# Kernel tuning notes

Hardware: AMD Instinct MI355X
Metric: run time of the kernel (lower is better)

## Reference

```python
import jax, jax.numpy as jnp
import numpy as np

DIM, HEADS, DIM_HEAD = 1024, 16, 64
INNER = HEADS * DIM_HEAD
EPS = 1e-5

def layernorm(x, w, b):
    mu = jnp.mean(x, axis=-1, keepdims=True)
    var = jnp.var(x, axis=-1, keepdims=True)
    return (x - mu) / jnp.sqrt(var + EPS) * w + b

def setup_inputs() -> dict:
    key = jax.random.key(0)
    ks = jax.random.split(key, 8)
    s = lambda d: 1.0 / np.sqrt(d)
    return {
        'x': jax.random.normal(ks[0], (4, 2048, DIM), jnp.float32),
        'media': jax.random.normal(ks[1], (4, 1024, DIM), jnp.float32),
        'ln_w': jnp.ones((DIM,), jnp.float32),
        'ln_b': jnp.zeros((DIM,), jnp.float32),
        'Wq': jax.random.normal(ks[2], (DIM, INNER), jnp.float32) * s(DIM),
        'Wkv': jax.random.normal(ks[3], (DIM, 2 * INNER), jnp.float32) * s(DIM),
        'Wo': jax.random.normal(ks[4], (INNER, DIM), jnp.float32) * s(INNER),
        'attn_gate': jnp.zeros((1,), jnp.float32),
        'ffln_w': jnp.ones((DIM,), jnp.float32),
        'ffln_b': jnp.zeros((DIM,), jnp.float32),
        'W1': jax.random.normal(ks[5], (DIM, 4 * DIM), jnp.float32) * s(DIM),
        'W2': jax.random.normal(ks[6], (4 * DIM, DIM), jnp.float32) * s(4 * DIM),
    }

def reference(x, media, ln_w, ln_b, Wq, Wkv, Wo, attn_gate, ffln_w, ffln_b, W1, W2):
    scale = DIM_HEAD ** (-0.5)
    b, n, _ = x.shape
    m = media.shape[1]
    # MaskedCrossAttention
    xn = layernorm(x, ln_w, ln_b)
    q = (xn @ Wq).reshape(b, n, HEADS, DIM_HEAD).transpose(0, 2, 1, 3)  # b h n d
    kv = media @ Wkv
    k, v = jnp.split(kv, 2, axis=-1)
    k = k.reshape(b, m, HEADS, DIM_HEAD).transpose(0, 2, 1, 3)  # b h m d
    v = v.reshape(b, m, HEADS, DIM_HEAD).transpose(0, 2, 1, 3)
    sim = jnp.einsum('bhid,bhjd->bhij', q * scale, k)
    # original subtracts detached row-max then softmax: identical to stable softmax
    attn = jax.nn.softmax(sim, axis=-1)
    out = jnp.einsum('bhij,bhjd->bhid', attn, v)
    out = out.transpose(0, 2, 1, 3).reshape(b, n, INNER) @ Wo
    x = out * jnp.tanh(attn_gate) + x
    # FeedForward (note: ff_gate exists in module but is unused in forward)
    h = layernorm(x, ffln_w, ffln_b) @ W1
    h = jax.nn.gelu(h, approximate=False) @ W2
    return h + x
```

## Files before the change

### kernel.cpp

```cpp
#include <hip/hip_runtime.h>
#include <hip/hip_bf16.h>

using bf16 = __hip_bfloat16;
typedef __attribute__((ext_vector_type(8))) short short8;
typedef __attribute__((ext_vector_type(4))) float f32x4;

typedef const void __attribute__((address_space(1))) gvoid;
typedef void __attribute__((address_space(3))) svoid;

__device__ __forceinline__ f32x4 mfma16(short8 a, short8 b, f32x4 c) {
    return __builtin_amdgcn_mfma_f32_16x16x32_bf16(a, b, c, 0, 0, 0);
}

__device__ __forceinline__ void async16(void* lds, const void* g) {
    __builtin_amdgcn_global_load_lds((gvoid*)g, (svoid*)lds, 16, 0, 0);
}

__device__ __forceinline__ unsigned short f2b(float f) {
    bf16 h = __float2bfloat16(f);
    unsigned short u;
    __builtin_memcpy(&u, &h, 2);
    return u;
}

__device__ __forceinline__ float fast_gelu(float x) {
    const float z0 = fmaf(x * x * x, 0.1029432f, 2.3022083f * x);
    const float z = fminf(z0, 80.0f);
    const float e = __builtin_amdgcn_exp2f(z);
    return x * e / (1.0f + e);
}

__global__ __launch_bounds__(256) void prep(
    const float* __restrict__ Wq, const float* __restrict__ Wkv,
    const float* __restrict__ Wo, const float* __restrict__ W1,
    const float* __restrict__ W2, bf16* __restrict__ WqT, bf16* __restrict__ WkvT,
    bf16* __restrict__ WoT, bf16* __restrict__ W1T, bf16* __restrict__ W2T,
    const float* __restrict__ media, bf16* __restrict__ mediab,
    const float* __restrict__ gate, float* __restrict__ gatet) {
    int id = blockIdx.x;
    const float* in;
    bf16* outp;
    int K, N, bx, by;
    if (id < 1024) {
        in = Wq; outp = WqT; K = 1024; N = 1024; bx = id & 31; by = id >> 5;
    } else if (id < 3072) {
        id -= 1024; in = Wkv; outp = WkvT; K = 1024; N = 2048; bx = id & 63; by = id >> 6;
    } else if (id < 4096) {
        id -= 3072; in = Wo; outp = WoT; K = 1024; N = 1024; bx = id & 31; by = id >> 5;
    } else if (id < 8192) {
        id -= 4096; in = W1; outp = W1T; K = 1024; N = 4096; bx = id & 127; by = id >> 7;
    } else if (id < 12288) {
        id -= 8192; in = W2; outp = W2T; K = 4096; N = 1024; bx = id & 31; by = id >> 5;
    } else {
        if (blockIdx.x == 12288 && threadIdx.x == 0) gatet[0] = tanhf(gate[0]);
        id -= 12288;
        const size_t i = (size_t)id * 256 + threadIdx.x;
        float4 v = ((const float4*)media)[i];
        ushort4 o;
        o.x = f2b(v.x); o.y = f2b(v.y); o.z = f2b(v.z); o.w = f2b(v.w);
        ((ushort4*)mediab)[i] = o;
        return;
    }
    __shared__ float tile[32][33];
    const int tx = threadIdx.x & 31, ty = threadIdx.x >> 5;
    const int n0 = bx * 32, k0 = by * 32;
#pragma unroll
    for (int j = 0; j < 32; j += 8)
        tile[ty + j][tx] = in[(size_t)(k0 + ty + j) * N + n0 + tx];
    __syncthreads();
#pragma unroll
    for (int j = 0; j < 32; j += 8)
        outp[(size_t)(n0 + ty + j) * K + k0 + tx] = __float2bfloat16(tile[tx][ty + j]);
}

__global__ __launch_bounds__(256) void layernorm_bf16(
    const float* __restrict__ x, const float* __restrict__ w,
    const float* __restrict__ b, bf16* __restrict__ out) {
    const int row = blockIdx.x, t = threadIdx.x;
    const float4 v = ((const float4*)(x + (size_t)row * 1024))[t];
    float s = v.x + v.y + v.z + v.w;
    float s2 = v.x * v.x + v.y * v.y + v.z * v.z + v.w * v.w;
#pragma unroll
    for (int off = 1; off < 64; off <<= 1) {
        s += __shfl_xor(s, off);
        s2 += __shfl_xor(s2, off);
    }
    __shared__ float rs[4], rs2[4];
    if ((t & 63) == 0) { rs[t >> 6] = s; rs2[t >> 6] = s2; }
    __syncthreads();
    const float S = rs[0] + rs[1] + rs[2] + rs[3];
    const float S2 = rs2[0] + rs2[1] + rs2[2] + rs2[3];
    const float mean = S * (1.0f / 1024.0f);
    const float var = S2 * (1.0f / 1024.0f) - mean * mean;
    const float rstd = rsqrtf(var + 1e-5f);
    const float4 wv = ((const float4*)w)[t];
    const float4 bv = ((const float4*)b)[t];
    ushort4 o;
    o.x = f2b((v.x - mean) * rstd * wv.x + bv.x);
    o.y = f2b((v.y - mean) * rstd * wv.y + bv.y);
    o.z = f2b((v.z - mean) * rstd * wv.z + bv.z);
    o.w = f2b((v.w - mean) * rstd * wv.w + bv.w);
    ((ushort4*)(out + (size_t)row * 1024))[t] = o;
}

__global__ __launch_bounds__(256) void vtranspose(
    const bf16* __restrict__ kvb, bf16* __restrict__ vtg) {
    const int mt = blockIdx.x, bh = blockIdx.y;
    const int b = bh >> 4, h = bh & 15;
    const int m0 = mt * 64;
    __shared__ bf16 tile[64 * 72];
    const int t = threadIdx.x;
#pragma unroll
    for (int i = 0; i < 2; ++i) {
        const int m = i * 32 + (t >> 3);
        short8 v = *(const short8*)(kvb + ((size_t)b * 1024 + m0 + m) * 2048 + 1024 +
                                    (size_t)h * 64 + (t & 7) * 8);
        *(short8*)&tile[m * 72 + (t & 7) * 8] = v;
    }
    __syncthreads();
#pragma unroll
    for (int i = 0; i < 2; ++i) {
        const int d = i * 32 + (t >> 3);
        const int mb = (t & 7) * 8;
        bf16 tmp[8];
#pragma unroll
        for (int j = 0; j < 8; ++j) tmp[j] = tile[(mb + j) * 72 + d];
        *(short8*)(vtg + (size_t)bh * 65536 + (size_t)d * 1024 + m0 + mb) = *(short8*)tmp;
    }
}

enum { EPI_BF16 = 0, EPI_GELU = 1, EPI_GATE_RES = 2, EPI_RES = 3 };

template <int EPI>
__global__ __launch_bounds__(256) void gemm_bf16(
    const bf16* __restrict__ A, const bf16* __restrict__ BT, void* __restrict__ Cout,
    const float* __restrict__ res, const float* __restrict__ gate_p,
    int M, int N, int K) {
    __shared__ bf16 As[128 * 64];
    __shared__ bf16 Bs[128 * 64];
    const int t = threadIdx.x;
    const int lane = t & 63;
    const int quad = lane >> 4, l15 = lane & 15;
    const int wave = t >> 6;
    const int wm = (wave >> 1) * 64, wn = (wave & 1) * 64;
    const int bm = blockIdx.x * 128, bn = blockIdx.y * 128;

    const int sr = t >> 3;
    const int sc = (t & 7) ^ (sr & 7);
    const bf16* Ag = A + (size_t)(bm + sr) * K + sc * 8;
    const bf16* Bg = BT + (size_t)(bn + sr) * K + sc * 8;

    f32x4 acc[4][4] = {};

    for (int k0 = 0; k0 < K; k0 += 64) {
#pragma unroll
        for (int i = 0; i < 4; ++i) {
            async16(&As[i * 2048 + t * 8], Ag + (size_t)i * 32 * K + k0);
            async16(&Bs[i * 2048 + t * 8], Bg + (size_t)i * 32 * K + k0);
        }
        __syncthreads();

#pragma unroll
        for (int dk = 0; dk < 2; ++dk) {
            short8 af[4], bf[4];
#pragma unroll
            for (int i = 0; i < 4; ++i)
                af[i] = *(const short8*)&As[(wm + i * 16 + l15) * 64 +
                                            (((dk * 4 + quad) ^ (l15 & 7)) * 8)];
#pragma unroll
            for (int i = 0; i < 4; ++i)
                bf[i] = *(const short8*)&Bs[(wn + i * 16 + l15) * 64 +
                                            (((dk * 4 + quad) ^ (l15 & 7)) * 8)];
#pragma unroll
            for (int i = 0; i < 4; ++i)
#pragma unroll
                for (int j = 0; j < 4; ++j)
                    acc[i][j] = mfma16(af[i], bf[j], acc[i][j]);
        }
        __syncthreads();
    }

    const float gate = (EPI == EPI_GATE_RES) ? gate_p[0] : 0.0f;
#pragma unroll
    for (int i = 0; i < 4; ++i) {
#pragma unroll
        for (int j = 0; j < 4; ++j) {
#pragma unroll
            for (int r = 0; r < 4; ++r) {
                const int row = bm + wm + i * 16 + quad * 4 + r;
                const int col = bn + wn + j * 16 + l15;
                const size_t idx = (size_t)row * N + col;
                const float v = acc[i][j][r];
                if constexpr (EPI == EPI_BF16) {
                    ((bf16*)Cout)[idx] = __float2bfloat16(v);
                } else if constexpr (EPI == EPI_GELU) {
                    ((bf16*)Cout)[idx] = __float2bfloat16(fast_gelu(v));
                } else if constexpr (EPI == EPI_GATE_RES) {
                    ((float*)Cout)[idx] = gate * v + res[idx];
                } else {
                    ((float*)Cout)[idx] = v + res[idx];
                }
            }
        }
    }
}

__global__ __launch_bounds__(256) void attention(
    const bf16* __restrict__ q, const bf16* __restrict__ kvb,
    const bf16* __restrict__ vtg, bf16* __restrict__ out) {
    const int bh = blockIdx.y;
    const int b = bh >> 4, h = bh & 15;
    const int t = threadIdx.x;
    const int wave = t >> 6, lane = t & 63;
    const int quad = lane >> 4, l15 = lane & 15;
    const int qrow0 = blockIdx.x * 128 + wave * 32;

    __shared__ bf16 Ks[128 * 64];
    __shared__ bf16 Vts[64 * 128];
    __shared__ bf16 Ps[4][16 * 128];

    short8 qa[2][2];
    const size_t qbase = ((size_t)b * 2048 + qrow0) * 1024 + (size_t)h * 64;
#pragma unroll
    for (int g = 0; g < 2; ++g)
#pragma unroll
        for (int dk = 0; dk < 2; ++dk)
            qa[g][dk] = *(const short8*)(q + qbase + (size_t)(g * 16 + l15) * 1024 + dk * 32 + quad * 8);

    f32x4 o[2][4] = {};
    float lsum[2][4] = {};

    const int km = t >> 3;
    const int kc = (t & 7) ^ (km & 7);
    const bf16* ksrc = kvb + ((size_t)b * 1024 + km) * 2048 + (size_t)h * 64 + kc * 8;
    const int vd = t >> 4;
    const int vc = (t & 15) ^ vd;
    const bf16* vsrc = vtg + (size_t)bh * 65536 + (size_t)vd * 1024 + vc * 8;

    bf16* Pw = &Ps[wave][0];

    for (int m0 = 0; m0 < 1024; m0 += 128) {
        __syncthreads();
#pragma unroll
        for (int i = 0; i < 4; ++i) {
            async16(&Ks[i * 2048 + t * 8], ksrc + ((size_t)m0 + i * 32) * 2048);
            async16(&Vts[i * 2048 + t * 8], vsrc + (size_t)i * 16 * 1024 + m0);
        }
        __syncthreads();

#pragma unroll
        for (int g = 0; g < 2; ++g) {
#pragma unroll
            for (int mt = 0; mt < 8; ++mt) {
                f32x4 s = {};
#pragma unroll
                for (int dk = 0; dk < 2; ++dk) {
                    short8 kb = *(const short8*)&Ks[(mt * 16 + l15) * 64 +
                                                    (((dk * 4 + quad) ^ (l15 & 7)) * 8)];
                    s = mfma16(qa[g][dk], kb, s);
                }
                const int pc = mt * 2 + (l15 >> 3);
                const int pj = l15 & 7;
#pragma unroll
                for (int r = 0; r < 4; ++r) {
                    const int row = quad * 4 + r;
                    const float p = __builtin_amdgcn_exp2f(
                        fmaf(s[r], 0.18033688f, -11.5415603f));
                    lsum[g][r] += p;
                    Pw[row * 128 + ((pc ^ row) & 15) * 8 + pj] = __float2bfloat16(p);
                }
            }
            asm volatile("s_waitcnt lgkmcnt(0)" ::: "memory");

#pragma unroll
            for (int ks = 0; ks < 4; ++ks) {
                short8 pa = *(const short8*)&Pw[l15 * 128 + (((ks * 4 + quad) ^ l15) & 15) * 8];
#pragma unroll
                for (int nt = 0; nt < 4; ++nt) {
                    short8 vb = *(const short8*)&Vts[(nt * 16 + l15) * 128 +
                                                     (((ks * 4 + quad) ^ l15) & 15) * 8];
                    o[g][nt] = mfma16(pa, vb, o[g][nt]);
                }
            }
            asm volatile("s_waitcnt lgkmcnt(0)" ::: "memory");
        }
    }

#pragma unroll
    for (int g = 0; g < 2; ++g)
#pragma unroll
        for (int r = 0; r < 4; ++r) {
            float ls = lsum[g][r];
#pragma unroll
            for (int d = 1; d < 16; d <<= 1) ls += __shfl_xor(ls, d);
            lsum[g][r] = 1.0f / ls;
        }

#pragma unroll
    for (int g = 0; g < 2; ++g)
#pragma unroll
        for (int nt = 0; nt < 4; ++nt)
#pragma unroll
            for (int r = 0; r < 4; ++r)
                out[((size_t)b * 2048 + qrow0 + g * 16 + quad * 4 + r) * 1024 +
                    (size_t)h * 64 + nt * 16 + l15] =
                    __float2bfloat16(o[g][nt][r] * lsum[g][r]);
}


extern "C" void kernel_launch(void* const* d_in, const int* in_sizes, int n_in,
                              void* d_out, int out_size, void* d_ws, size_t ws_size,
                              hipStream_t stream) {
    const float* x    = (const float*)d_in[0];
    const float* media= (const float*)d_in[1];
    const float* ln_w = (const float*)d_in[2];
    const float* ln_b = (const float*)d_in[3];
    const float* Wq   = (const float*)d_in[4];
    const float* Wkv  = (const float*)d_in[5];
    const float* Wo   = (const float*)d_in[6];
    const float* gate = (const float*)d_in[7];
    const float* ffw  = (const float*)d_in[8];
    const float* ffb  = (const float*)d_in[9];
    const float* W1   = (const float*)d_in[10];
    const float* W2   = (const float*)d_in[11];
    float* out = (float*)d_out;

    char* p = (char*)d_ws;
    bf16* WqT    = (bf16*)p;               p += (size_t)1024 * 1024 * 2;
    bf16* WkvT   = (bf16*)p;               p += (size_t)2048 * 1024 * 2;
    bf16* WoT    = (bf16*)p;               p += (size_t)1024 * 1024 * 2;
    bf16* W1T    = (bf16*)p;               p += (size_t)4096 * 1024 * 2;
    bf16* W2T    = (bf16*)p;               p += (size_t)1024 * 4096 * 2;
    bf16* xn     = (bf16*)p;               p += (size_t)8192 * 1024 * 2;
    bf16* mediab = (bf16*)p;               p += (size_t)4096 * 1024 * 2;
    bf16* qb     = (bf16*)p;               p += (size_t)8192 * 1024 * 2;
    bf16* kvb    = (bf16*)p;               p += (size_t)4096 * 2048 * 2;
    bf16* vtg    = (bf16*)p;               p += (size_t)64 * 64 * 1024 * 2;
    bf16* attnb  = (bf16*)p;               p += (size_t)8192 * 1024 * 2;
    bf16* hb     = (bf16*)p;               p += (size_t)8192 * 4096 * 2;
    float* x2    = (float*)p;              p += (size_t)8192 * 1024 * 4;
    float* gatet = (float*)p;              p += 256;
    bf16* x2n = xn;

    prep<<<16384, 256, 0, stream>>>(Wq, Wkv, Wo, W1, W2, WqT, WkvT, WoT, W1T, W2T,
                                    media, mediab, gate, gatet);

    layernorm_bf16<<<8192, 256, 0, stream>>>(x, ln_w, ln_b, xn);
    gemm_bf16<EPI_BF16><<<dim3(64, 8), 256, 0, stream>>>(xn, WqT, qb, nullptr, nullptr, 8192, 1024, 1024);
    gemm_bf16<EPI_BF16><<<dim3(32, 16), 256, 0, stream>>>(mediab, WkvT, kvb, nullptr, nullptr, 4096, 2048, 1024);
    vtranspose<<<dim3(16, 64), 256, 0, stream>>>(kvb, vtg);
    attention<<<dim3(16, 64), 256, 0, stream>>>(qb, kvb, vtg, attnb);
    gemm_bf16<EPI_GATE_RES><<<dim3(64, 8), 256, 0, stream>>>(attnb, WoT, x2, x, gatet, 8192, 1024, 1024);

    layernorm_bf16<<<8192, 256, 0, stream>>>(x2, ffw, ffb, x2n);
    gemm_bf16<EPI_GELU><<<dim3(64, 32), 256, 0, stream>>>(x2n, W1T, hb, nullptr, nullptr, 8192, 4096, 1024);
    gemm_bf16<EPI_RES><<<dim3(64, 8), 256, 0, stream>>>(hb, W2T, out, x2, nullptr, 8192, 1024, 4096);
}
```

Baseline: 494.4 us.

## Double-buffer GEMM LDS tiles with async prefetch and enlarge block to 256x128

The bf16 GEMM now uses 512-thread blocks computing 256x128 tiles, with two LDS buffers per operand. The next K-tiles are prefetched by async global-to-LDS loads and gated by vmcnt waits, so global loads overlap with MFMA work. MFMA sections also get raised wave priority, and all LDS fragment loads are issued before the MFMAs. The costs are doubled LDS use (96KB per block), which limits occupancy, and fewer blocks per GEMM.

```diff
diff --git a/kernel.cpp b/kernel.cpp
--- a/kernel.cpp
+++ b/kernel.cpp
@@ -132,18 +132,18 @@
 enum { EPI_BF16 = 0, EPI_GELU = 1, EPI_GATE_RES = 2, EPI_RES = 3 };
 
 template <int EPI>
-__global__ __launch_bounds__(256) void gemm_bf16(
+__global__ __launch_bounds__(512, 2) void gemm_bf16(
     const bf16* __restrict__ A, const bf16* __restrict__ BT, void* __restrict__ Cout,
     const float* __restrict__ res, const float* __restrict__ gate_p,
     int M, int N, int K) {
-    __shared__ bf16 As[128 * 64];
-    __shared__ bf16 Bs[128 * 64];
+    __shared__ bf16 As[2][256 * 64];
+    __shared__ bf16 Bs[2][128 * 64];
     const int t = threadIdx.x;
     const int lane = t & 63;
     const int quad = lane >> 4, l15 = lane & 15;
     const int wave = t >> 6;
     const int wm = (wave >> 1) * 64, wn = (wave & 1) * 64;
-    const int bm = blockIdx.x * 128, bn = blockIdx.y * 128;
+    const int bm = blockIdx.x * 256, bn = blockIdx.y * 128;
 
     const int sr = t >> 3;
     const int sc = (t & 7) ^ (sr & 7);
@@ -152,32 +152,63 @@
 
     f32x4 acc[4][4] = {};
 
-    for (int k0 = 0; k0 < K; k0 += 64) {
-#pragma unroll
-        for (int i = 0; i < 4; ++i) {
-            async16(&As[i * 2048 + t * 8], Ag + (size_t)i * 32 * K + k0);
-            async16(&Bs[i * 2048 + t * 8], Bg + (size_t)i * 32 * K + k0);
-        }
-        __syncthreads();
-
-#pragma unroll
-        for (int dk = 0; dk < 2; ++dk) {
-            short8 af[4], bf[4];
-#pragma unroll
-            for (int i = 0; i < 4; ++i)
-                af[i] = *(const short8*)&As[(wm + i * 16 + l15) * 64 +
-                                            (((dk * 4 + quad) ^ (l15 & 7)) * 8)];
-#pragma unroll
-            for (int i = 0; i < 4; ++i)
-                bf[i] = *(const short8*)&Bs[(wn + i * 16 + l15) * 64 +
-                                            (((dk * 4 + quad) ^ (l15 & 7)) * 8)];
-#pragma unroll
-            for (int i = 0; i < 4; ++i)
-#pragma unroll
-                for (int j = 0; j < 4; ++j)
-                    acc[i][j] = mfma16(af[i], bf[j], acc[i][j]);
-        }
-        __syncthreads();
+    auto stage = [&](int buf, int k0) {
+#pragma unroll
+        for (int i = 0; i < 4; ++i)
+            async16(&As[buf][i * 4096 + t * 8], Ag + (size_t)i * 64 * K + k0);
+#pragma unroll
+        for (int i = 0; i < 2; ++i)
+            async16(&Bs[buf][i * 4096 + t * 8], Bg + (size_t)i * 64 * K + k0);
+    };
+
+    const int NT = K >> 6;
+    stage(0, 0);
+    stage(1, 64);
+
+    for (int tt = 0; tt < NT; ++tt) {
+        const int cur = tt & 1;
+        if (tt < NT - 1) {
+            asm volatile("s_waitcnt vmcnt(6)" ::: "memory");
+        } else {
+            asm volatile("s_waitcnt vmcnt(0)" ::: "memory");
+        }
+        __builtin_amdgcn_s_barrier();
+        __builtin_amdgcn_sched_barrier(0);
+
+        short8 a0[4], b0[4], a1[4], b1[4];
+#pragma unroll
+        for (int i = 0; i < 4; ++i)
+            a0[i] = *(const short8*)&As[cur][(wm + i * 16 + l15) * 64 +
+                                            ((quad ^ (l15 & 7)) * 8)];
+#pragma unroll
+        for (int j = 0; j < 4; ++j)
+            b0[j] = *(const short8*)&Bs[cur][(wn + j * 16 + l15) * 64 +
+                                            ((quad ^ (l15 & 7)) * 8)];
+#pragma unroll
+        for (int i = 0; i < 4; ++i)
+            a1[i] = *(const short8*)&As[cur][(wm + i * 16 + l15) * 64 +
+                                            (((4 + quad) ^ (l15 & 7)) * 8)];
+#pragma unroll
+        for (int j = 0; j < 4; ++j)
+            b1[j] = *(const short8*)&Bs[cur][(wn + j * 16 + l15) * 64 +
+                                            (((4 + quad) ^ (l15 & 7)) * 8)];
+
+        __builtin_amdgcn_s_setprio(1);
+#pragma unroll
+        for (int i = 0; i < 4; ++i)
+#pragma unroll
+            for (int j = 0; j < 4; ++j)
+                acc[i][j] = mfma16(a0[i], b0[j], acc[i][j]);
+#pragma unroll
+        for (int i = 0; i < 4; ++i)
+#pragma unroll
+            for (int j = 0; j < 4; ++j)
+                acc[i][j] = mfma16(a1[i], b1[j], acc[i][j]);
+        __builtin_amdgcn_s_setprio(0);
+
+        __builtin_amdgcn_sched_barrier(0);
+        __builtin_amdgcn_s_barrier();
+        if (tt + 2 < NT) stage(cur, (tt + 2) << 6);
     }
 
     const float gate = (EPI == EPI_GATE_RES) ? gate_p[0] : 0.0f;
@@ -346,13 +377,13 @@
                                     media, mediab, gate, gatet);
 
     layernorm_bf16<<<8192, 256, 0, stream>>>(x, ln_w, ln_b, xn);
-    gemm_bf16<EPI_BF16><<<dim3(64, 8), 256, 0, stream>>>(xn, WqT, qb, nullptr, nullptr, 8192, 1024, 1024);
-    gemm_bf16<EPI_BF16><<<dim3(32, 16), 256, 0, stream>>>(mediab, WkvT, kvb, nullptr, nullptr, 4096, 2048, 1024);
+    gemm_bf16<EPI_BF16><<<dim3(32, 8), 512, 0, stream>>>(xn, WqT, qb, nullptr, nullptr, 8192, 1024, 1024);
+    gemm_bf16<EPI_BF16><<<dim3(16, 16), 512, 0, stream>>>(mediab, WkvT, kvb, nullptr, nullptr, 4096, 2048, 1024);
     vtranspose<<<dim3(16, 64), 256, 0, stream>>>(kvb, vtg);
     attention<<<dim3(16, 64), 256, 0, stream>>>(qb, kvb, vtg, attnb);
-    gemm_bf16<EPI_GATE_RES><<<dim3(64, 8), 256, 0, stream>>>(attnb, WoT, x2, x, gatet, 8192, 1024, 1024);
+    gemm_bf16<EPI_GATE_RES><<<dim3(32, 8), 512, 0, stream>>>(attnb, WoT, x2, x, gatet, 8192, 1024, 1024);
 
     layernorm_bf16<<<8192, 256, 0, stream>>>(x2, ffw, ffb, x2n);
-    gemm_bf16<EPI_GELU><<<dim3(64, 32), 256, 0, stream>>>(x2n, W1T, hb, nullptr, nullptr, 8192, 4096, 1024);
-    gemm_bf16<EPI_RES><<<dim3(64, 8), 256, 0, stream>>>(hb, W2T, out, x2, nullptr, 8192, 1024, 4096);
-}
+    gemm_bf16<EPI_GELU><<<dim3(32, 32), 512, 0, stream>>>(x2n, W1T, hb, nullptr, nullptr, 8192, 4096, 1024);
+    gemm_bf16<EPI_RES><<<dim3(32, 8), 512, 0, stream>>>(hb, W2T, out, x2, nullptr, 8192, 1024, 4096);
+}
```

Measured after the change: 497.7 us. No clear change (+0.7%).
